# Kernel tuning notes

Measured on AMD Instinct MI355X. Metric: run time of the kernel, lower is better.

## Reference

```python
import jax, jax.numpy as jnp
import numpy as np

B = 2097152  # flattened batch of 3x3 rotation matrices

def setup_inputs() -> dict:
    key = jax.random.key(0)
    k1, k2 = jax.random.split(key)
    # scale by 0.1 so cos=(trace(m1 m2^T)-1)/2 stays strictly inside (-1,1)
    pred_rot = jax.random.normal(k1, (B, 3, 3), dtype=jnp.float32) * 0.1
    gt_rot = jax.random.normal(k2, (B, 3, 3), dtype=jnp.float32) * 0.1
    return {"pred_rot": pred_rot, "gt_rot": gt_rot}

def reference(pred_rot, gt_rot):
    m1 = pred_rot.reshape(-1, 3, 3)
    m2 = gt_rot.reshape(-1, 3, 3)
    # trace(m1 @ m2^T) == sum(m1 * m2) elementwise -> avoid the bmm
    cos = (jnp.einsum('bij,bij->b', m1, m2) - 1.0) * 0.5
    cos = jnp.clip(cos, -1.0, 1.0)  # min with +1, max with -1
    theta = jnp.arccos(cos)
    return jnp.mean(theta)  # reduction='mean'
```

## Files before the change

kernel.cpp:

```cpp
#include <hip/hip_runtime.h>
#include <math.h>


#define TPB 256
#define MPB 1024
#define F_PER_TILE 9216
#define F4_PER_TILE 2304
#define NBLOCKS 512

#define DECL(S)                                                             \
    float4 S##A0, S##A1, S##A2, S##A3, S##A4, S##A5, S##A6, S##A7, S##A8,   \
           S##B0, S##B1, S##B2, S##B3, S##B4, S##B5, S##B6, S##B7, S##B8;

#define LOADSET(S, t)                                                       \
    {                                                                       \
        const float4* __restrict__ pa = (const float4*)a + (t) * F4_PER_TILE + tid; \
        const float4* __restrict__ pb = (const float4*)b + (t) * F4_PER_TILE + tid; \
        S##A0 = pa[0];    S##A1 = pa[256];  S##A2 = pa[512];                \
        S##A3 = pa[768];  S##A4 = pa[1024]; S##A5 = pa[1280];               \
        S##A6 = pa[1536]; S##A7 = pa[1792]; S##A8 = pa[2048];               \
        S##B0 = pb[0];    S##B1 = pb[256];  S##B2 = pb[512];                \
        S##B3 = pb[768];  S##B4 = pb[1024]; S##B5 = pb[1280];               \
        S##B6 = pb[1536]; S##B7 = pb[1792]; S##B8 = pb[2048];               \
    }

#define PK(S, k)                                                            \
    {                                                                       \
        float4 p;                                                           \
        p.x = S##A##k.x * S##B##k.x; p.y = S##A##k.y * S##B##k.y;           \
        p.z = S##A##k.z * S##B##k.z; p.w = S##A##k.w * S##B##k.w;           \
        ((float4*)prod)[k * 256 + tid] = p;                                 \
    }

#define CONSUME(S)                                                          \
    {                                                                       \
        PK(S, 0) PK(S, 1) PK(S, 2) PK(S, 3) PK(S, 4)                        \
        PK(S, 5) PK(S, 6) PK(S, 7) PK(S, 8)                                 \
        __syncthreads();                                                    \
        _Pragma("unroll")                                                   \
        for (int c = 0; c < 4; ++c) {                                       \
            const int bsx = 9 * (tid + 256 * c);                            \
            float d = ((prod[bsx + 0] + prod[bsx + 1]) +                    \
                       (prod[bsx + 2] + prod[bsx + 3])) +                   \
                      ((prod[bsx + 4] + prod[bsx + 5]) +                    \
                       (prod[bsx + 6] + prod[bsx + 7])) + prod[bsx + 8];    \
            float cv = fminf(1.0f, fmaxf(-1.0f, (d - 1.0f) * 0.5f));        \
            sum += acosf(cv);                                               \
        }                                                                   \
        __syncthreads();                                                    \
    }

__global__ __launch_bounds__(TPB) void geo_kernel(
    const float* __restrict__ a, const float* __restrict__ b,
    float* __restrict__ out, float invM, int M)
{
    __shared__ float prod[F_PER_TILE];
    __shared__ float wsum[TPB / 64];

    const int tid = threadIdx.x;
    float sum = 0.0f;

    const long long ntf = (long long)M / MPB;
    DECL(X) DECL(Y)

    long long tile = blockIdx.x;
    if (tile < ntf) {
        LOADSET(X, tile)
        int phase = 0;
        for (;;) {
            const long long next = tile + gridDim.x;
            const bool more = (next < ntf);
            if (phase == 0) {
                if (more) LOADSET(Y, next)
                asm volatile("" ::: "memory");
                CONSUME(X)
            } else {
                if (more) LOADSET(X, next)
                asm volatile("" ::: "memory");
                CONSUME(Y)
            }
            if (!more) break;
            tile = next;
            phase ^= 1;
        }
    }

    {
        const long long gid    = (long long)blockIdx.x * TPB + tid;
        const long long stride = (long long)gridDim.x * TPB;
        for (long long m = ntf * MPB + gid; m < M; m += stride) {
            float d = 0.0f;
            for (int j = 0; j < 9; ++j)
                d = fmaf(a[m * 9 + j], b[m * 9 + j], d);
            float cv = fminf(1.0f, fmaxf(-1.0f, (d - 1.0f) * 0.5f));
            sum += acosf(cv);
        }
    }

    #pragma unroll
    for (int off = 32; off > 0; off >>= 1)
        sum += __shfl_down(sum, off, 64);
    const int lane = tid & 63;
    const int wid  = tid >> 6;
    if (lane == 0) wsum[wid] = sum;
    __syncthreads();
    if (tid == 0) {
        float s = 0.0f;
        #pragma unroll
        for (int i = 0; i < TPB / 64; ++i) s += wsum[i];
        atomicAdd(out, s * invM);
    }
}

extern "C" void kernel_launch(void* const* d_in, const int* in_sizes, int n_in,
                              void* d_out, int out_size, void* d_ws, size_t ws_size,
                              hipStream_t stream) {
    const float* a = (const float*)d_in[0];
    const float* b = (const float*)d_in[1];
    float* out = (float*)d_out;

    const int n = in_sizes[0];
    const int M = n / 9;

    hipMemsetAsync(out, 0, (size_t)out_size * sizeof(float), stream);
    geo_kernel<<<NBLOCKS, TPB, 0, stream>>>(a, b, out, 1.0f / (float)M, M);
}
```

Before: 165.0 us.

## Replace LDS-staged tiled pipeline with per-thread 4-matrix register reduction

Removes the shared-memory staging, the double-buffered register prefetch and the two barriers per tile. Each thread now loads 9 contiguous float4 from each input, covering 4 matrices, computes their dot products directly in registers with FMAs, and evaluates acos. The grid grows from 512 to 2048 blocks to supply memory-level parallelism through occupancy instead of explicit prefetch. The trade-off is that per-thread accesses are no longer coalesced across the wavefront: adjacent lanes read 144-byte strided chunks, which may cost more memory transactions.

```diff
diff --git a/kernel.cpp b/kernel.cpp
--- a/kernel.cpp
+++ b/kernel.cpp
@@ -3,98 +3,66 @@
 
 
 #define TPB 256
-#define MPB 1024
-#define F_PER_TILE 9216
-#define F4_PER_TILE 2304
-#define NBLOCKS 512
-
-#define DECL(S)                                                             \
-    float4 S##A0, S##A1, S##A2, S##A3, S##A4, S##A5, S##A6, S##A7, S##A8,   \
-           S##B0, S##B1, S##B2, S##B3, S##B4, S##B5, S##B6, S##B7, S##B8;
-
-#define LOADSET(S, t)                                                       \
-    {                                                                       \
-        const float4* __restrict__ pa = (const float4*)a + (t) * F4_PER_TILE + tid; \
-        const float4* __restrict__ pb = (const float4*)b + (t) * F4_PER_TILE + tid; \
-        S##A0 = pa[0];    S##A1 = pa[256];  S##A2 = pa[512];                \
-        S##A3 = pa[768];  S##A4 = pa[1024]; S##A5 = pa[1280];               \
-        S##A6 = pa[1536]; S##A7 = pa[1792]; S##A8 = pa[2048];               \
-        S##B0 = pb[0];    S##B1 = pb[256];  S##B2 = pb[512];                \
-        S##B3 = pb[768];  S##B4 = pb[1024]; S##B5 = pb[1280];               \
-        S##B6 = pb[1536]; S##B7 = pb[1792]; S##B8 = pb[2048];               \
-    }
-
-#define PK(S, k)                                                            \
-    {                                                                       \
-        float4 p;                                                           \
-        p.x = S##A##k.x * S##B##k.x; p.y = S##A##k.y * S##B##k.y;           \
-        p.z = S##A##k.z * S##B##k.z; p.w = S##A##k.w * S##B##k.w;           \
-        ((float4*)prod)[k * 256 + tid] = p;                                 \
-    }
-
-#define CONSUME(S)                                                          \
-    {                                                                       \
-        PK(S, 0) PK(S, 1) PK(S, 2) PK(S, 3) PK(S, 4)                        \
-        PK(S, 5) PK(S, 6) PK(S, 7) PK(S, 8)                                 \
-        __syncthreads();                                                    \
-        _Pragma("unroll")                                                   \
-        for (int c = 0; c < 4; ++c) {                                       \
-            const int bsx = 9 * (tid + 256 * c);                            \
-            float d = ((prod[bsx + 0] + prod[bsx + 1]) +                    \
-                       (prod[bsx + 2] + prod[bsx + 3])) +                   \
-                      ((prod[bsx + 4] + prod[bsx + 5]) +                    \
-                       (prod[bsx + 6] + prod[bsx + 7])) + prod[bsx + 8];    \
-            float cv = fminf(1.0f, fmaxf(-1.0f, (d - 1.0f) * 0.5f));        \
-            sum += acosf(cv);                                               \
-        }                                                                   \
-        __syncthreads();                                                    \
-    }
+#define NBLOCKS 2048
 
 __global__ __launch_bounds__(TPB) void geo_kernel(
     const float* __restrict__ a, const float* __restrict__ b,
     float* __restrict__ out, float invM, int M)
 {
-    __shared__ float prod[F_PER_TILE];
     __shared__ float wsum[TPB / 64];
-
     const int tid = threadIdx.x;
     float sum = 0.0f;
 
-    const long long ntf = (long long)M / MPB;
-    DECL(X) DECL(Y)
+    const long long G    = (long long)M >> 2;
+    const long long gid0 = (long long)blockIdx.x * TPB + tid;
+    const long long gstr = (long long)gridDim.x * TPB;
 
-    long long tile = blockIdx.x;
-    if (tile < ntf) {
-        LOADSET(X, tile)
-        int phase = 0;
-        for (;;) {
-            const long long next = tile + gridDim.x;
-            const bool more = (next < ntf);
-            if (phase == 0) {
-                if (more) LOADSET(Y, next)
-                asm volatile("" ::: "memory");
-                CONSUME(X)
-            } else {
-                if (more) LOADSET(X, next)
-                asm volatile("" ::: "memory");
-                CONSUME(Y)
-            }
-            if (!more) break;
-            tile = next;
-            phase ^= 1;
-        }
+    for (long long g = gid0; g < G; g += gstr) {
+        const float4* __restrict__ pa = (const float4*)a + 9 * g;
+        const float4* __restrict__ pb = (const float4*)b + 9 * g;
+        const float4 A0 = pa[0], A1 = pa[1], A2 = pa[2], A3 = pa[3], A4 = pa[4],
+                     A5 = pa[5], A6 = pa[6], A7 = pa[7], A8 = pa[8];
+        const float4 B0 = pb[0], B1 = pb[1], B2 = pb[2], B3 = pb[3], B4 = pb[4],
+                     B5 = pb[5], B6 = pb[6], B7 = pb[7], B8 = pb[8];
+
+        float d0 = A0.x * B0.x;
+        d0 = fmaf(A0.y, B0.y, d0); d0 = fmaf(A0.z, B0.z, d0);
+        d0 = fmaf(A0.w, B0.w, d0);
+        d0 = fmaf(A1.x, B1.x, d0); d0 = fmaf(A1.y, B1.y, d0);
+        d0 = fmaf(A1.z, B1.z, d0); d0 = fmaf(A1.w, B1.w, d0);
+        d0 = fmaf(A2.x, B2.x, d0);
+
+        float d1 = A2.y * B2.y;
+        d1 = fmaf(A2.z, B2.z, d1); d1 = fmaf(A2.w, B2.w, d1);
+        d1 = fmaf(A3.x, B3.x, d1); d1 = fmaf(A3.y, B3.y, d1);
+        d1 = fmaf(A3.z, B3.z, d1); d1 = fmaf(A3.w, B3.w, d1);
+        d1 = fmaf(A4.x, B4.x, d1); d1 = fmaf(A4.y, B4.y, d1);
+
+        float d2 = A4.z * B4.z;
+        d2 = fmaf(A4.w, B4.w, d2);
+        d2 = fmaf(A5.x, B5.x, d2); d2 = fmaf(A5.y, B5.y, d2);
+        d2 = fmaf(A5.z, B5.z, d2); d2 = fmaf(A5.w, B5.w, d2);
+        d2 = fmaf(A6.x, B6.x, d2); d2 = fmaf(A6.y, B6.y, d2);
+        d2 = fmaf(A6.z, B6.z, d2);
+
+        float d3 = A6.w * B6.w;
+        d3 = fmaf(A7.x, B7.x, d3); d3 = fmaf(A7.y, B7.y, d3);
+        d3 = fmaf(A7.z, B7.z, d3); d3 = fmaf(A7.w, B7.w, d3);
+        d3 = fmaf(A8.x, B8.x, d3); d3 = fmaf(A8.y, B8.y, d3);
+        d3 = fmaf(A8.z, B8.z, d3); d3 = fmaf(A8.w, B8.w, d3);
+
+        sum += acosf(fminf(1.0f, fmaxf(-1.0f, (d0 - 1.0f) * 0.5f)));
+        sum += acosf(fminf(1.0f, fmaxf(-1.0f, (d1 - 1.0f) * 0.5f)));
+        sum += acosf(fminf(1.0f, fmaxf(-1.0f, (d2 - 1.0f) * 0.5f)));
+        sum += acosf(fminf(1.0f, fmaxf(-1.0f, (d3 - 1.0f) * 0.5f)));
     }
 
-    {
-        const long long gid    = (long long)blockIdx.x * TPB + tid;
-        const long long stride = (long long)gridDim.x * TPB;
-        for (long long m = ntf * MPB + gid; m < M; m += stride) {
-            float d = 0.0f;
-            for (int j = 0; j < 9; ++j)
-                d = fmaf(a[m * 9 + j], b[m * 9 + j], d);
-            float cv = fminf(1.0f, fmaxf(-1.0f, (d - 1.0f) * 0.5f));
-            sum += acosf(cv);
-        }
+    for (long long m = 4 * G + gid0; m < M; m += gstr) {
+        float d = 0.0f;
+        #pragma unroll
+        for (int j = 0; j < 9; ++j)
+            d = fmaf(a[m * 9 + j], b[m * 9 + j], d);
+        sum += acosf(fminf(1.0f, fmaxf(-1.0f, (d - 1.0f) * 0.5f)));
     }
 
     #pragma unroll
```

Result: slower. 169.7 us (+2.9%).
